# Kernel tuning notes

Measured on AMD Instinct MI355X. Metric: run time of the kernel, lower is better.

The kernel has to match this reference:

```python
import jax, jax.numpy as jnp
import numpy as np
from jax import lax

BN_EPS = 1e-5

def _conv(x, w, b, stride=2, pad=1):
    y = lax.conv_general_dilated(x, w, (stride, stride), [(pad, pad), (pad, pad)],
                                 dimension_numbers=('NCHW', 'OIHW', 'NCHW'))
    return y + b[None, :, None, None]

def _leaky(x):
    return jnp.where(x >= 0, x, 0.2 * x)

def setup_inputs() -> dict:
    key = jax.random.key(0)
    ks = jax.random.split(key, 10)
    B, C, S = 64, 3, 128
    flat = 128 * (S // 4) * (S // 4)  # 131072
    out_f, kdims = 100, 5
    def kaiming(k, shape, fan_in):
        bound = 1.0 / np.sqrt(fan_in)
        return jax.random.uniform(k, shape, jnp.float32, -bound, bound)
    x = jax.random.normal(ks[0], (B, C, S, S), jnp.float32)
    conv1_w = kaiming(ks[1], (64, C, 4, 4), C * 16)
    conv1_b = kaiming(ks[2], (64,), C * 16)
    conv2_w = kaiming(ks[3], (128, 64, 4, 4), 64 * 16)
    conv2_b = kaiming(ks[4], (128,), 64 * 16)
    bn_gamma = jnp.ones((128,), jnp.float32)
    bn_beta = jnp.zeros((128,), jnp.float32)
    T = jax.random.normal(ks[5], (flat, out_f, kdims), jnp.float32)  # N(0,1) init
    lin_w = kaiming(ks[6], (1, flat + out_f), flat + out_f)
    lin_b = kaiming(ks[7], (1,), flat + out_f)
    return {"x": x, "conv1_w": conv1_w, "conv1_b": conv1_b,
            "conv2_w": conv2_w, "conv2_b": conv2_b,
            "bn_gamma": bn_gamma, "bn_beta": bn_beta,
            "T": T, "lin_w": lin_w, "lin_b": lin_b}

def reference(x, conv1_w, conv1_b, conv2_w, conv2_b, bn_gamma, bn_beta, T, lin_w, lin_b):
    B = x.shape[0]
    h = _leaky(_conv(x, conv1_w, conv1_b))          # [B,64,S/2,S/2]
    h = _conv(h, conv2_w, conv2_b)                  # [B,128,S/4,S/4]
    mu = jnp.mean(h, axis=(0, 2, 3), keepdims=True)  # batchnorm (train mode, batch stats)
    var = jnp.mean((h - mu) ** 2, axis=(0, 2, 3), keepdims=True)
    h = (h - mu) * lax.rsqrt(var + BN_EPS)
    h = h * bn_gamma[None, :, None, None] + bn_beta[None, :, None, None]
    h = _leaky(h)
    feat = h.reshape(B, -1)                          # [B, flat]
    # minibatch discrimination
    M = (feat @ T.reshape(T.shape[0], -1)).reshape(B, T.shape[1], T.shape[2])  # [B,out,k]
    norm = jnp.abs(M[None, :, :, :] - M[:, None, :, :]).sum(3)  # [B,B,out] pairwise L1
    o_b = jnp.exp(-norm).sum(0)                      # [B,out]
    feat = jnp.concatenate([feat, o_b], axis=1)      # [B, flat+out]
    logits = feat @ lin_w.T + lin_b
    return jax.nn.sigmoid(logits)                    # [B,1]
```

## Files before the change

kernel.cpp:

```cpp
#include <hip/hip_runtime.h>
#include <hip/hip_bf16.h>
#include <math.h>

#define BB 64
#define SS 128
#define C1 64
#define H1D 64
#define C2 128
#define H2D 32
#define FLAT 131072
#define NCOL 500
#define KCH 256
#define KCSZ 512

typedef __attribute__((ext_vector_type(4))) float f32x4;
typedef __attribute__((ext_vector_type(8))) short bf16x8;

__device__ inline float bf2f(short s) {
    union { unsigned int u; float f; } z;
    z.u = ((unsigned int)(unsigned short)s) << 16;
    return z.f;
}

__device__ inline void bn_coeff(const double* __restrict__ bnp,
    const float* __restrict__ gamma, const float* __restrict__ beta,
    int c, float& sc, float& sh)
{
    double s1 = 0.0, s2 = 0.0;
    #pragma unroll
    for (int s = 0; s < 8; s++) { s1 += bnp[c*8+s]; s2 += bnp[1024 + c*8+s]; }
    double mean = s1 * (1.0/65536.0);
    double var  = s2 * (1.0/65536.0) - mean*mean;
    double rstd = 1.0 / sqrt(var + 1e-5);
    double scd  = rstd * (double)gamma[c];
    sc = (float)scd;
    sh = (float)((double)beta[c] - mean*scd);
}

__global__ __launch_bounds__(256) void k_conv1p(const float* __restrict__ x,
    const float* __restrict__ w, const float* __restrict__ bias,
    const float* __restrict__ w2,
    __hip_bfloat16* __restrict__ h1, __hip_bfloat16* __restrict__ Bw)
{
    int bid = blockIdx.x;
    if (bid < 512) {
      int i = bid*256 + threadIdx.x;
      int jj = i & 7, oc = (i>>3)&127, kl8 = (i>>10)&31, stage = i>>15;
      int kl = kl8*8 + jj;
      int tap = kl >> 4, icl = kl & 15;
      int ic = stage*16 + icl;
      Bw[i] = __float2bfloat16(w2[(size_t)oc*1024 + ic*16 + tap]);
      return;
    }
    int tid = (bid - 512)*256 + threadIdx.x;
    int ow = tid & 63, oh = (tid>>6)&63, bi = tid>>12;
    int ih0 = oh*2-1, iw0 = ow*2-1;
    float in[48];
    #pragma unroll
    for (int ic=0; ic<3; ic++)
      #pragma unroll
      for (int kh=0; kh<4; kh++)
        #pragma unroll
        for (int kw=0; kw<4; kw++) {
          int ih = ih0+kh, iw = iw0+kw;
          float v = 0.f;
          if ((unsigned)ih < 128u && (unsigned)iw < 128u)
            v = x[((size_t)(bi*3+ic)*SS + ih)*SS + iw];
          in[ic*16+kh*4+kw] = v;
        }
    #pragma unroll
    for (int g=0; g<4; g++) {
      __hip_bfloat16 outv[16];
      #pragma unroll
      for (int ocl=0; ocl<16; ocl++) {
        int oc = g*16 + ocl;
        float a = bias[oc];
        const float* wp = w + oc*48;
        #pragma unroll
        for (int t=0; t<48; t++) a = fmaf(in[t], wp[t], a);
        a = a >= 0.f ? a : 0.2f*a;
        outv[ocl] = __float2bfloat16(a);
      }
      __hip_bfloat16* dst = h1 + (((size_t)g*BB + bi)*4096 + oh*64 + ow)*16;
      *(bf16x8*)(dst)     = *(bf16x8*)&outv[0];
      *(bf16x8*)(dst + 8) = *(bf16x8*)&outv[8];
    }
}

__global__ __launch_bounds__(256) void k_conv2(const __hip_bfloat16* __restrict__ h1,
    const __hip_bfloat16* __restrict__ Bw, const float* __restrict__ b2,
    __hip_bfloat16* __restrict__ h2b)
{
    int bx = blockIdx.x;
    int nh = bx & 1, strip = (bx>>1)&3, bi = bx>>3;
    int lane = threadIdx.x & 63, wv = threadIdx.x >> 6;
    int l15 = lane & 15, kg = lane >> 4;

    __shared__ __align__(16) short tile[36*33*24];

    f32x4 acc[4][4];
    #pragma unroll
    for (int m=0;m<4;m++)
      #pragma unroll
      for (int n=0;n<4;n++) acc[m][n] = (f32x4)(0.f);

    int ihb = strip*16 - 1;

    for (int stage=0; stage<4; ++stage) {
      const __hip_bfloat16* hsrc = h1 + ((size_t)stage*BB + bi)*4096*16;
      for (int idx = threadIdx.x; idx < 2376; idx += 256) {
        int half = idx & 1, p = idx >> 1;
        int ih_l = p / 66, iw_l = p - ih_l*66;
        int ih = ihb + ih_l, iw = iw_l - 1;
        int row48 = (ih_l*2 + (iw_l&1))*33 + (iw_l>>1);
        bf16x8 v = (bf16x8)(0);
        if ((unsigned)ih < 64u && (unsigned)iw < 64u)
          v = *(const bf16x8*)(hsrc + ((size_t)(ih*64+iw)*16 + half*8));
        *(bf16x8*)&tile[row48*24 + half*8] = v;
      }
      __syncthreads();
      const __hip_bfloat16* bwst = Bw + (size_t)stage*32*128*8;
      #pragma unroll
      for (int j=0; j<8; j++) {
        bf16x8 bf[4];
        #pragma unroll
        for (int nf=0; nf<4; nf++)
          bf[nf] = *(const bf16x8*)(bwst + ((size_t)((j*4+kg)*128) + nh*64 + nf*16 + l15)*8);
        int tap = 2*j + (kg>>1);
        int kh = tap>>2, kw = tap&3;
        int icl0 = (kg&1)*8;
        bf16x8 af[4];
        #pragma unroll
        for (int mf=0; mf<4; mf++) {
          int oh_l = 2*wv + (mf>>1);
          int ow   = (mf&1)*16 + l15;
          int ih_l = 2*oh_l + kh;
          int iw_l = 2*ow + kw;
          int row48 = (ih_l*2 + (iw_l&1))*33 + (iw_l>>1);
          af[mf] = *(const bf16x8*)&tile[row48*24 + icl0];
        }
        #pragma unroll
        for (int mf=0; mf<4; mf++)
          #pragma unroll
          for (int nf=0; nf<4; nf++)
            acc[mf][nf] = __builtin_amdgcn_mfma_f32_16x16x32_bf16(af[mf], bf[nf], acc[mf][nf], 0, 0, 0);
      }
      __syncthreads();
    }
    #pragma unroll
    for (int mf=0; mf<4; mf++)
      #pragma unroll
      for (int nf=0; nf<4; nf++) {
        int oc = nh*64 + nf*16 + l15;
        int p0 = wv*64 + mf*16 + kg*4;
        float bv = b2[oc];
        __hip_bfloat16 o4[4];
        o4[0] = __float2bfloat16(acc[mf][nf][0] + bv);
        o4[1] = __float2bfloat16(acc[mf][nf][1] + bv);
        o4[2] = __float2bfloat16(acc[mf][nf][2] + bv);
        o4[3] = __float2bfloat16(acc[mf][nf][3] + bv);
        *(double*)&h2b[((size_t)bi*C2 + oc)*1024 + strip*256 + p0] = *(double*)o4;
      }
}

__global__ __launch_bounds__(256) void k_bnstats1(const __hip_bfloat16* __restrict__ h2b,
    double* __restrict__ bnp)
{
    int c = blockIdx.x & 127, s = blockIdx.x >> 7;
    double s1 = 0.0, s2 = 0.0;
    for (int g = threadIdx.x; g < 1024; g += 256) {
      int b = s*8 + (g >> 7), hw8 = g & 127;
      bf16x8 v = *(const bf16x8*)&h2b[((size_t)b*C2 + c)*1024 + hw8*8];
      #pragma unroll
      for (int j=0;j<8;j++) {
        double f = (double)bf2f(v[j]);
        s1 += f; s2 = fma(f, f, s2);
      }
    }
    __shared__ double r1[256], r2[256];
    r1[threadIdx.x] = s1; r2[threadIdx.x] = s2;
    __syncthreads();
    for (int st = 128; st > 0; st >>= 1) {
      if (threadIdx.x < st) { r1[threadIdx.x] += r1[threadIdx.x+st]; r2[threadIdx.x] += r2[threadIdx.x+st]; }
      __syncthreads();
    }
    if (threadIdx.x == 0) {
      bnp[c*8 + s]        = r1[0];
      bnp[1024 + c*8 + s] = r2[0];
    }
}

__global__ __launch_bounds__(256) void k_mgemm(const __hip_bfloat16* __restrict__ h2b,
    const double* __restrict__ bnp, const float* __restrict__ gamma,
    const float* __restrict__ beta, const float* __restrict__ T,
    __hip_bfloat16* __restrict__ Mpart)
{
    int t = threadIdx.x;
    int lane = t & 63, wv = t >> 6;
    int l15 = lane & 15, kg = lane >> 4;
    int bid = blockIdx.x;
    int xc = bid & 7, j = bid >> 3;
    int kc = xc*32 + (j >> 2);
    int ng = j & 3;
    int k0b = kc * KCSZ;

    float sc, sh;
    bn_coeff(bnp, gamma, beta, kc >> 1, sc, sh);

    __shared__ float Ts[2][32][134];

    int f4c = t & 31, rbase = t >> 5;
    int cols4 = ng*128 + f4c*4;
    bool cvalid = cols4 < 500;

    f32x4 acc[4][2];
    #pragma unroll
    for (int m=0;m<4;m++) { acc[m][0] = (f32x4)(0.f); acc[m][1] = (f32x4)(0.f); }

    float4 tv0, tv1, tv2, tv3;
    {
      int ks0 = k0b;
      tv0 = cvalid ? *(const float4*)&T[(size_t)(ks0+rbase   )*NCOL + cols4] : make_float4(0,0,0,0);
      tv1 = cvalid ? *(const float4*)&T[(size_t)(ks0+rbase+ 8)*NCOL + cols4] : make_float4(0,0,0,0);
      tv2 = cvalid ? *(const float4*)&T[(size_t)(ks0+rbase+16)*NCOL + cols4] : make_float4(0,0,0,0);
      tv3 = cvalid ? *(const float4*)&T[(size_t)(ks0+rbase+24)*NCOL + cols4] : make_float4(0,0,0,0);
      float* d0 = &Ts[0][rbase   ][f4c*4];
      float* d1 = &Ts[0][rbase+ 8][f4c*4];
      float* d2 = &Ts[0][rbase+16][f4c*4];
      float* d3 = &Ts[0][rbase+24][f4c*4];
      *(float2*)d0 = make_float2(tv0.x,tv0.y); *(float2*)(d0+2) = make_float2(tv0.z,tv0.w);
      *(float2*)d1 = make_float2(tv1.x,tv1.y); *(float2*)(d1+2) = make_float2(tv1.z,tv1.w);
      *(float2*)d2 = make_float2(tv2.x,tv2.y); *(float2*)(d2+2) = make_float2(tv2.z,tv2.w);
      *(float2*)d3 = make_float2(tv3.x,tv3.y); *(float2*)(d3+2) = make_float2(tv3.z,tv3.w);
    }
    __syncthreads();

    for (int s = 0; s < 16; s++) {
      int cur = s & 1;
      if (s < 15) {
        int ks0 = k0b + (s+1)*32;
        tv0 = cvalid ? *(const float4*)&T[(size_t)(ks0+rbase   )*NCOL + cols4] : make_float4(0,0,0,0);
        tv1 = cvalid ? *(const float4*)&T[(size_t)(ks0+rbase+ 8)*NCOL + cols4] : make_float4(0,0,0,0);
        tv2 = cvalid ? *(const float4*)&T[(size_t)(ks0+rbase+16)*NCOL + cols4] : make_float4(0,0,0,0);
        tv3 = cvalid ? *(const float4*)&T[(size_t)(ks0+rbase+24)*NCOL + cols4] : make_float4(0,0,0,0);
      }
      {
        int k0 = k0b + s*32;
        bf16x8 af[4];
        #pragma unroll
        for (int mf=0; mf<4; mf++) {
          bf16x8 raw = *(const bf16x8*)(h2b + (size_t)(mf*16 + l15)*FLAT + k0 + kg*8);
          __hip_bfloat16 ta[8];
          #pragma unroll
          for (int jj=0; jj<8; jj++) {
            float f = fmaf(bf2f(raw[jj]), sc, sh);
            f = f >= 0.f ? f : 0.2f*f;
            ta[jj] = __float2bfloat16(f);
          }
          af[mf] = *(bf16x8*)ta;
        }
        bf16x8 bfr[2];
        #pragma unroll
        for (int nf=0; nf<2; nf++) {
          int c = wv*32 + nf*16 + l15;
          __hip_bfloat16 tb[8];
          #pragma unroll
          for (int jj=0; jj<8; jj++)
            tb[jj] = __float2bfloat16(Ts[cur][kg*8+jj][c]);
          bfr[nf] = *(bf16x8*)tb;
        }
        #pragma unroll
        for (int mf=0;mf<4;mf++)
          #pragma unroll
          for (int nf=0;nf<2;nf++)
            acc[mf][nf] = __builtin_amdgcn_mfma_f32_16x16x32_bf16(af[mf], bfr[nf], acc[mf][nf], 0, 0, 0);
      }
      __syncthreads();
      if (s < 15) {
        int nb = cur ^ 1;
        float* d0 = &Ts[nb][rbase   ][f4c*4];
        float* d1 = &Ts[nb][rbase+ 8][f4c*4];
        float* d2 = &Ts[nb][rbase+16][f4c*4];
        float* d3 = &Ts[nb][rbase+24][f4c*4];
        *(float2*)d0 = make_float2(tv0.x,tv0.y); *(float2*)(d0+2) = make_float2(tv0.z,tv0.w);
        *(float2*)d1 = make_float2(tv1.x,tv1.y); *(float2*)(d1+2) = make_float2(tv1.z,tv1.w);
        *(float2*)d2 = make_float2(tv2.x,tv2.y); *(float2*)(d2+2) = make_float2(tv2.z,tv2.w);
        *(float2*)d3 = make_float2(tv3.x,tv3.y); *(float2*)(d3+2) = make_float2(tv3.z,tv3.w);
        __syncthreads();
      }
    }
    __hip_bfloat16* op = Mpart + (size_t)(kc*4 + ng)*8192;
    #pragma unroll
    for (int mf=0; mf<4; mf++) {
      __hip_bfloat16 buf[8];
      #pragma unroll
      for (int nf=0; nf<2; nf++)
        #pragma unroll
        for (int q=0; q<4; q++)
          buf[nf*4+q] = __float2bfloat16(acc[mf][nf][q]);
      *(bf16x8*)(op + ((size_t)mf*256 + t)*8) = *(bf16x8*)buf;
    }
}

__global__ __launch_bounds__(256) void k_mreduce(const __hip_bfloat16* __restrict__ Mpart,
    float* __restrict__ M)
{
    int i = blockIdx.x*256 + threadIdx.x;
    int r = i / NCOL, c = i - r*NCOL;
    int mf = r >> 4, kg = (r >> 2) & 3, q = r & 3;
    int ng = c >> 7, wv = (c >> 5) & 3, nf = (c >> 4) & 1, l15 = c & 15;
    int t = wv*64 + kg*16 + l15;
    const __hip_bfloat16* p = Mpart + ((size_t)ng*1024 + mf*256 + t)*8 + nf*4 + q;
    float s = 0.f;
    #pragma unroll 8
    for (int kc = 0; kc < KCH; kc++) s += __bfloat162float(p[(size_t)kc*32768]);
    M[i] = s;
}

__global__ __launch_bounds__(256) void k_ob(const float* __restrict__ M,
    float* __restrict__ ob)
{
    int o = blockIdx.x;
    __shared__ float Ms[320];
    __shared__ float red[256];
    for (int idx = threadIdx.x; idx < 320; idx += 256) {
      int a = idx / 5, d = idx - a*5;
      Ms[idx] = M[(size_t)a*NCOL + o*5 + d];
    }
    __syncthreads();
    int b = threadIdx.x & 63, aq = threadIdx.x >> 6;
    float s = 0.f;
    for (int a = aq*16; a < aq*16+16; a++) {
      float n = 0.f;
      #pragma unroll
      for (int d=0; d<5; d++) n += fabsf(Ms[a*5+d] - Ms[b*5+d]);
      s += expf(-n);
    }
    red[threadIdx.x] = s;
    __syncthreads();
    if (threadIdx.x < 64)
      ob[(size_t)b*100 + o] = red[b] + red[64+b] + red[128+b] + red[192+b];
}

__global__ __launch_bounds__(256) void k_final1(const __hip_bfloat16* __restrict__ h2b,
    const double* __restrict__ bnp, const float* __restrict__ gamma,
    const float* __restrict__ beta, const float* __restrict__ lw,
    double* __restrict__ fpart)
{
    int bx = blockIdx.x;
    int b = bx >> 3, s = bx & 7;
    __shared__ float scs[16], shs[16];
    if (threadIdx.x < 16) {
      float sc, sh;
      bn_coeff(bnp, gamma, beta, s*16 + threadIdx.x, sc, sh);
      scs[threadIdx.x] = sc; shs[threadIdx.x] = sh;
    }
    __syncthreads();
    const __hip_bfloat16* hp = h2b + (size_t)b*FLAT;
    double acc = 0.0;
    for (int g = s*2048 + threadIdx.x; g < (s+1)*2048; g += 256) {
      int k = g*8;
      int cl = (k >> 10) & 15;
      float sc = scs[cl], sh = shs[cl];
      bf16x8 v = *(const bf16x8*)&hp[k];
      float4 w0 = *(const float4*)&lw[k];
      float4 w1 = *(const float4*)&lw[k+4];
      float f0 = fmaf(bf2f(v[0]), sc, sh); f0 = f0>=0.f?f0:0.2f*f0;
      float f1 = fmaf(bf2f(v[1]), sc, sh); f1 = f1>=0.f?f1:0.2f*f1;
      float f2 = fmaf(bf2f(v[2]), sc, sh); f2 = f2>=0.f?f2:0.2f*f2;
      float f3 = fmaf(bf2f(v[3]), sc, sh); f3 = f3>=0.f?f3:0.2f*f3;
      float f4 = fmaf(bf2f(v[4]), sc, sh); f4 = f4>=0.f?f4:0.2f*f4;
      float f5 = fmaf(bf2f(v[5]), sc, sh); f5 = f5>=0.f?f5:0.2f*f5;
      float f6 = fmaf(bf2f(v[6]), sc, sh); f6 = f6>=0.f?f6:0.2f*f6;
      float f7 = fmaf(bf2f(v[7]), sc, sh); f7 = f7>=0.f?f7:0.2f*f7;
      acc = fma((double)f0, (double)w0.x, acc);
      acc = fma((double)f1, (double)w0.y, acc);
      acc = fma((double)f2, (double)w0.z, acc);
      acc = fma((double)f3, (double)w0.w, acc);
      acc = fma((double)f4, (double)w1.x, acc);
      acc = fma((double)f5, (double)w1.y, acc);
      acc = fma((double)f6, (double)w1.z, acc);
      acc = fma((double)f7, (double)w1.w, acc);
    }
    __shared__ double red[256];
    red[threadIdx.x] = acc;
    __syncthreads();
    for (int st = 128; st > 0; st >>= 1) {
      if (threadIdx.x < st) red[threadIdx.x] += red[threadIdx.x + st];
      __syncthreads();
    }
    if (threadIdx.x == 0) fpart[bx] = red[0];
}

__global__ void k_final2(const double* __restrict__ fpart,
    const float* __restrict__ ob, const float* __restrict__ lw,
    const float* __restrict__ lb, float* __restrict__ out)
{
    int b = threadIdx.x;
    double s = 0.0;
    #pragma unroll
    for (int i = 0; i < 8; i++) s += fpart[b*8 + i];
    for (int o = 0; o < 100; o++)
      s = fma((double)ob[(size_t)b*100 + o], (double)lw[FLAT + o], s);
    s += (double)lb[0];
    out[b] = (float)(1.0 / (1.0 + exp(-s)));
}

extern "C" void kernel_launch(void* const* d_in, const int* in_sizes, int n_in,
                              void* d_out, int out_size, void* d_ws, size_t ws_size,
                              hipStream_t stream)
{
    const float* x   = (const float*)d_in[0];
    const float* w1  = (const float*)d_in[1];
    const float* b1  = (const float*)d_in[2];
    const float* w2  = (const float*)d_in[3];
    const float* b2  = (const float*)d_in[4];
    const float* gam = (const float*)d_in[5];
    const float* bet = (const float*)d_in[6];
    const float* T   = (const float*)d_in[7];
    const float* lw  = (const float*)d_in[8];
    const float* lb  = (const float*)d_in[9];
    float* out = (float*)d_out;

    float* ws = (float*)d_ws;
    __hip_bfloat16* h1 = (__hip_bfloat16*)ws;
    __hip_bfloat16* Mpart = (__hip_bfloat16*)ws;
    __hip_bfloat16* h2b = (__hip_bfloat16*)(ws + 8388608);
    __hip_bfloat16* Bw  = (__hip_bfloat16*)(ws + 12582912);
    float* M     = ws + 12582912 + 65536;
    float* ob    = M + 32000;
    double* bnp   = (double*)(ob + 6400);
    double* fpart = bnp + 2048;

    k_conv1p<<<1536, 256, 0, stream>>>(x, w1, b1, w2, h1, Bw);
    k_conv2<<<512, 256, 0, stream>>>(h1, Bw, b2, h2b);
    k_bnstats1<<<1024, 256, 0, stream>>>(h2b, bnp);
    k_mgemm<<<1024, 256, 0, stream>>>(h2b, bnp, gam, bet, T, Mpart);
    k_mreduce<<<125, 256, 0, stream>>>(Mpart, M);
    k_ob<<<100, 256, 0, stream>>>(M, ob);
    k_final1<<<512, 256, 0, stream>>>(h2b, bnp, gam, bet, lw, fpart);
    k_final2<<<1, 64, 0, stream>>>(fpart, ob, lw, lb, out);
}
```

Before: 178.8 us.

## Fuse BN statistics into conv2 epilogue and split M reduction into coalesced stages

conv2 now accumulates per-channel sum and sum-of-squares from its fp32 accumulators in its epilogue and writes per-block partials. A small reduction kernel turns these into scale/shift once, so the separate stats pass that re-read h2 is gone and downstream kernels no longer recompute the BN coefficients. The strided M reduction over 256 chunks becomes a coalesced vectorized partial sum over groups of 8 chunks, with the last 32-way sum folded into k_ob. Statistics are now taken from fp32 pre-rounding values rather than bf16-rounded ones, and the conv2 block index mapping changes.

```diff
diff --git a/kernel.cpp b/kernel.cpp
--- a/kernel.cpp
+++ b/kernel.cpp
@@ -22,21 +22,6 @@
     return z.f;
 }
 
-__device__ inline void bn_coeff(const double* __restrict__ bnp,
-    const float* __restrict__ gamma, const float* __restrict__ beta,
-    int c, float& sc, float& sh)
-{
-    double s1 = 0.0, s2 = 0.0;
-    #pragma unroll
-    for (int s = 0; s < 8; s++) { s1 += bnp[c*8+s]; s2 += bnp[1024 + c*8+s]; }
-    double mean = s1 * (1.0/65536.0);
-    double var  = s2 * (1.0/65536.0) - mean*mean;
-    double rstd = 1.0 / sqrt(var + 1e-5);
-    double scd  = rstd * (double)gamma[c];
-    sc = (float)scd;
-    sh = (float)((double)beta[c] - mean*scd);
-}
-
 __global__ __launch_bounds__(256) void k_conv1p(const float* __restrict__ x,
     const float* __restrict__ w, const float* __restrict__ bias,
     const float* __restrict__ w2,
@@ -89,14 +74,17 @@
 
 __global__ __launch_bounds__(256) void k_conv2(const __hip_bfloat16* __restrict__ h1,
     const __hip_bfloat16* __restrict__ Bw, const float* __restrict__ b2,
-    __hip_bfloat16* __restrict__ h2b)
-{
-    int bx = blockIdx.x;
-    int nh = bx & 1, strip = (bx>>1)&3, bi = bx>>3;
+    __hip_bfloat16* __restrict__ h2b, double* __restrict__ bnp2)
+{
+    int bid = blockIdx.x;
+    int nh = (bid >> 3) & 1;
+    int pair = (bid >> 4)*8 + (bid & 7);
+    int bi = pair >> 2, strip = pair & 3;
     int lane = threadIdx.x & 63, wv = threadIdx.x >> 6;
     int l15 = lane & 15, kg = lane >> 4;
 
     __shared__ __align__(16) short tile[36*33*24];
+    __shared__ float2 bnl[4][16][16];
 
     f32x4 acc[4][4];
     #pragma unroll
@@ -148,51 +136,68 @@
       __syncthreads();
     }
     #pragma unroll
-    for (int mf=0; mf<4; mf++)
-      #pragma unroll
-      for (int nf=0; nf<4; nf++) {
-        int oc = nh*64 + nf*16 + l15;
+    for (int nf=0; nf<4; nf++) {
+      int oc = nh*64 + nf*16 + l15;
+      float bv = b2[oc];
+      float s1 = 0.f, s2 = 0.f;
+      #pragma unroll
+      for (int mf=0; mf<4; mf++) {
         int p0 = wv*64 + mf*16 + kg*4;
-        float bv = b2[oc];
+        float v0 = acc[mf][nf][0] + bv;
+        float v1 = acc[mf][nf][1] + bv;
+        float v2 = acc[mf][nf][2] + bv;
+        float v3 = acc[mf][nf][3] + bv;
+        s1 += v0+v1+v2+v3;
+        s2 = fmaf(v0,v0, fmaf(v1,v1, fmaf(v2,v2, fmaf(v3,v3, s2))));
         __hip_bfloat16 o4[4];
-        o4[0] = __float2bfloat16(acc[mf][nf][0] + bv);
-        o4[1] = __float2bfloat16(acc[mf][nf][1] + bv);
-        o4[2] = __float2bfloat16(acc[mf][nf][2] + bv);
-        o4[3] = __float2bfloat16(acc[mf][nf][3] + bv);
+        o4[0] = __float2bfloat16(v0); o4[1] = __float2bfloat16(v1);
+        o4[2] = __float2bfloat16(v2); o4[3] = __float2bfloat16(v3);
         *(double*)&h2b[((size_t)bi*C2 + oc)*1024 + strip*256 + p0] = *(double*)o4;
       }
-}
-
-__global__ __launch_bounds__(256) void k_bnstats1(const __hip_bfloat16* __restrict__ h2b,
-    double* __restrict__ bnp)
-{
-    int c = blockIdx.x & 127, s = blockIdx.x >> 7;
-    double s1 = 0.0, s2 = 0.0;
-    for (int g = threadIdx.x; g < 1024; g += 256) {
-      int b = s*8 + (g >> 7), hw8 = g & 127;
-      bf16x8 v = *(const bf16x8*)&h2b[((size_t)b*C2 + c)*1024 + hw8*8];
-      #pragma unroll
-      for (int j=0;j<8;j++) {
-        double f = (double)bf2f(v[j]);
-        s1 += f; s2 = fma(f, f, s2);
-      }
-    }
+      bnl[nf][wv*4+kg][l15] = make_float2(s1, s2);
+    }
+    __syncthreads();
+    if (threadIdx.x < 64) {
+      int nf = threadIdx.x >> 4, l = threadIdx.x & 15;
+      double s1 = 0.0, s2 = 0.0;
+      #pragma unroll
+      for (int i=0;i<16;i++) {
+        float2 v = bnl[nf][i][l];
+        s1 += (double)v.x; s2 += (double)v.y;
+      }
+      int oc = nh*64 + nf*16 + l;
+      bnp2[(size_t)oc*256 + pair]         = s1;
+      bnp2[32768 + (size_t)oc*256 + pair] = s2;
+    }
+}
+
+__global__ __launch_bounds__(256) void k_bnred(const double* __restrict__ bnp2,
+    const float* __restrict__ gamma, const float* __restrict__ beta,
+    float* __restrict__ stats)
+{
+    int c = blockIdx.x;
+    int p = threadIdx.x;
+    double s1 = bnp2[(size_t)c*256 + p];
+    double s2 = bnp2[32768 + (size_t)c*256 + p];
     __shared__ double r1[256], r2[256];
-    r1[threadIdx.x] = s1; r2[threadIdx.x] = s2;
+    r1[p] = s1; r2[p] = s2;
     __syncthreads();
     for (int st = 128; st > 0; st >>= 1) {
-      if (threadIdx.x < st) { r1[threadIdx.x] += r1[threadIdx.x+st]; r2[threadIdx.x] += r2[threadIdx.x+st]; }
+      if (p < st) { r1[p] += r1[p+st]; r2[p] += r2[p+st]; }
       __syncthreads();
     }
-    if (threadIdx.x == 0) {
-      bnp[c*8 + s]        = r1[0];
-      bnp[1024 + c*8 + s] = r2[0];
+    if (p == 0) {
+      double mean = r1[0] * (1.0/65536.0);
+      double var  = r2[0] * (1.0/65536.0) - mean*mean;
+      double rstd = 1.0 / sqrt(var + 1e-5);
+      double sc = rstd * (double)gamma[c];
+      stats[c]       = (float)sc;
+      stats[C2 + c]  = (float)((double)beta[c] - mean*sc);
     }
 }
 
 __global__ __launch_bounds__(256) void k_mgemm(const __hip_bfloat16* __restrict__ h2b,
-    const double* __restrict__ bnp, const float* __restrict__ gamma,
-    const float* __restrict__ beta, const float* __restrict__ T,
+    const float* __restrict__ stats, const float* __restrict__ T,
     __hip_bfloat16* __restrict__ Mpart)
 {
     int t = threadIdx.x;
@@ -204,8 +209,8 @@
     int ng = j & 3;
     int k0b = kc * KCSZ;
 
-    float sc, sh;
-    bn_coeff(bnp, gamma, beta, kc >> 1, sc, sh);
+    int ch = kc >> 1;
+    float sc = stats[ch], sh = stats[C2 + ch];
 
     __shared__ float Ts[2][32][134];
 
@@ -302,22 +307,36 @@
     }
 }
 
-__global__ __launch_bounds__(256) void k_mreduce(const __hip_bfloat16* __restrict__ Mpart,
-    float* __restrict__ M)
-{
-    int i = blockIdx.x*256 + threadIdx.x;
-    int r = i / NCOL, c = i - r*NCOL;
-    int mf = r >> 4, kg = (r >> 2) & 3, q = r & 3;
-    int ng = c >> 7, wv = (c >> 5) & 3, nf = (c >> 4) & 1, l15 = c & 15;
-    int t = wv*64 + kg*16 + l15;
-    const __hip_bfloat16* p = Mpart + ((size_t)ng*1024 + mf*256 + t)*8 + nf*4 + q;
-    float s = 0.f;
-    #pragma unroll 8
-    for (int kc = 0; kc < KCH; kc++) s += __bfloat162float(p[(size_t)kc*32768]);
-    M[i] = s;
-}
-
-__global__ __launch_bounds__(256) void k_ob(const float* __restrict__ M,
+__global__ __launch_bounds__(256) void k_mreduceA(const __hip_bfloat16* __restrict__ Mpart,
+    float* __restrict__ Mpart2)
+{
+    int ng = blockIdx.x & 3, kg8 = blockIdx.x >> 2;
+    int t = threadIdx.x;
+    f32x4 a0[4], a1[4];
+    #pragma unroll
+    for (int mf=0; mf<4; mf++) { a0[mf] = (f32x4)(0.f); a1[mf] = (f32x4)(0.f); }
+    #pragma unroll
+    for (int kcl=0; kcl<8; kcl++) {
+      int kc = kg8*8 + kcl;
+      const __hip_bfloat16* ch = Mpart + (size_t)(kc*4 + ng)*8192;
+      #pragma unroll
+      for (int mf=0; mf<4; mf++) {
+        bf16x8 v = *(const bf16x8*)(ch + ((size_t)mf*256 + t)*8);
+        a0[mf][0] += bf2f(v[0]); a0[mf][1] += bf2f(v[1]);
+        a0[mf][2] += bf2f(v[2]); a0[mf][3] += bf2f(v[3]);
+        a1[mf][0] += bf2f(v[4]); a1[mf][1] += bf2f(v[5]);
+        a1[mf][2] += bf2f(v[6]); a1[mf][3] += bf2f(v[7]);
+      }
+    }
+    #pragma unroll
+    for (int mf=0; mf<4; mf++) {
+      float* dst = Mpart2 + ((size_t)(ng*32 + kg8)*4 + mf)*2048 + t*8;
+      *(f32x4*)dst = a0[mf];
+      *(f32x4*)(dst+4) = a1[mf];
+    }
+}
+
+__global__ __launch_bounds__(256) void k_ob(const float* __restrict__ Mpart2,
     float* __restrict__ ob)
 {
     int o = blockIdx.x;
@@ -325,7 +344,15 @@
     __shared__ float red[256];
     for (int idx = threadIdx.x; idx < 320; idx += 256) {
       int a = idx / 5, d = idx - a*5;
-      Ms[idx] = M[(size_t)a*NCOL + o*5 + d];
+      int r = a, c = o*5 + d;
+      int mf = r >> 4, kg = (r >> 2) & 3, q = r & 3;
+      int ng = c >> 7, wv = (c >> 5) & 3, nf = (c >> 4) & 1, l15 = c & 15;
+      int t = wv*64 + kg*16 + l15, j8 = nf*4 + q;
+      const float* p = Mpart2 + ((size_t)(ng*32)*4 + mf)*2048 + t*8 + j8;
+      float s = 0.f;
+      #pragma unroll 8
+      for (int kg8 = 0; kg8 < 32; kg8++) s += p[(size_t)kg8*8192];
+      Ms[idx] = s;
     }
     __syncthreads();
     int b = threadIdx.x & 63, aq = threadIdx.x >> 6;
@@ -343,17 +370,15 @@
 }
 
 __global__ __launch_bounds__(256) void k_final1(const __hip_bfloat16* __restrict__ h2b,
-    const double* __restrict__ bnp, const float* __restrict__ gamma,
-    const float* __restrict__ beta, const float* __restrict__ lw,
+    const float* __restrict__ stats, const float* __restrict__ lw,
     double* __restrict__ fpart)
 {
     int bx = blockIdx.x;
     int b = bx >> 3, s = bx & 7;
     __shared__ float scs[16], shs[16];
     if (threadIdx.x < 16) {
-      float sc, sh;
-      bn_coeff(bnp, gamma, beta, s*16 + threadIdx.x, sc, sh);
-      scs[threadIdx.x] = sc; shs[threadIdx.x] = sh;
+      scs[threadIdx.x] = stats[s*16 + threadIdx.x];
+      shs[threadIdx.x] = stats[C2 + s*16 + threadIdx.x];
     }
     __syncthreads();
     const __hip_bfloat16* hp = h2b + (size_t)b*FLAT;
@@ -427,17 +452,18 @@
     __hip_bfloat16* Mpart = (__hip_bfloat16*)ws;
     __hip_bfloat16* h2b = (__hip_bfloat16*)(ws + 8388608);
     __hip_bfloat16* Bw  = (__hip_bfloat16*)(ws + 12582912);
-    float* M     = ws + 12582912 + 65536;
-    float* ob    = M + 32000;
-    double* bnp   = (double*)(ob + 6400);
-    double* fpart = bnp + 2048;
+    float* stats = ws + 12648448;
+    float* ob    = ws + 12648704;
+    float* Mpart2 = ws + 12655104;
+    double* bnp2  = (double*)(ws + 13703680);
+    double* fpart = (double*)(ws + 13834752);
 
     k_conv1p<<<1536, 256, 0, stream>>>(x, w1, b1, w2, h1, Bw);
-    k_conv2<<<512, 256, 0, stream>>>(h1, Bw, b2, h2b);
-    k_bnstats1<<<1024, 256, 0, stream>>>(h2b, bnp);
-    k_mgemm<<<1024, 256, 0, stream>>>(h2b, bnp, gam, bet, T, Mpart);
-    k_mreduce<<<125, 256, 0, stream>>>(Mpart, M);
-    k_ob<<<100, 256, 0, stream>>>(M, ob);
-    k_final1<<<512, 256, 0, stream>>>(h2b, bnp, gam, bet, lw, fpart);
+    k_conv2<<<512, 256, 0, stream>>>(h1, Bw, b2, h2b, bnp2);
+    k_bnred<<<128, 256, 0, stream>>>(bnp2, gam, bet, stats);
+    k_mgemm<<<1024, 256, 0, stream>>>(h2b, stats, T, Mpart);
+    k_mreduceA<<<128, 256, 0, stream>>>(Mpart, Mpart2);
+    k_ob<<<100, 256, 0, stream>>>(Mpart2, ob);
+    k_final1<<<512, 256, 0, stream>>>(h2b, stats, lw, fpart);
     k_final2<<<1, 64, 0, stream>>>(fpart, ob, lw, lb, out);
 }
```

Result: faster. 167.8 us (-6.2%).
